# Kernel tuning notes

Hardware: AMD Instinct MI355X
Metric: run time of the kernel (lower is better)

Reference implementation:

```python
import jax, jax.numpy as jnp
import numpy as np

HIDDEN = 1024
HEAD_DIM = 64
N_HEADS = HIDDEN // HEAD_DIM  # 16
BATCH = 2
SEQ = 2048
ROT_DIM = HEAD_DIM // 2  # RotaryEmbedding(head_dim // 2): only first half of head dims rotated
THETA = 10000.0
SCALE_BASE = 512.0  # lucidrains xpos default
EPS = 1e-5


def setup_inputs() -> dict:
    key = jax.random.key(0)
    ks = jax.random.split(key, 8)

    def lin(k, shape, fan_in):
        b = 1.0 / np.sqrt(fan_in)
        return jax.random.uniform(k, shape, jnp.float32, -b, b)

    return {
        "x": jax.random.normal(ks[0], (BATCH, SEQ, HIDDEN), jnp.float32),
        "ln1_w": jnp.ones((HIDDEN,), jnp.float32),
        "ln1_b": jnp.zeros((HIDDEN,), jnp.float32),
        "wqkv_w": lin(ks[1], (HIDDEN, 3 * HIDDEN), HIDDEN),
        "wg_w": lin(ks[2], (HIDDEN, HIDDEN), HIDDEN),
        "wo_w": lin(ks[3], (HIDDEN, HIDDEN), HIDDEN),
        "gn_w": jnp.ones((N_HEADS,), jnp.float32),
        "gn_b": jnp.zeros((N_HEADS,), jnp.float32),
        "ln2_w": jnp.ones((HIDDEN,), jnp.float32),
        "ln2_b": jnp.zeros((HIDDEN,), jnp.float32),
        "w1_w": lin(ks[4], (HIDDEN, HIDDEN), HIDDEN),
        "w1_b": lin(ks[5], (HIDDEN,), HIDDEN),
        "w2_w": lin(ks[6], (HIDDEN, HIDDEN), HIDDEN),
        "w2_b": lin(ks[7], (HIDDEN,), HIDDEN),
    }


def _layernorm(x, w, b):
    m = jnp.mean(x, axis=-1, keepdims=True)
    v = jnp.mean(jnp.square(x - m), axis=-1, keepdims=True)
    return (x - m) * jax.lax.rsqrt(v + EPS) * w + b


def _rotate_half(x):
    # interleaved pairs: (d r) with r=2 -> (-x2, x1)
    xs = x.reshape(x.shape[:-1] + (ROT_DIM // 2, 2))
    x1, x2 = xs[..., 0], xs[..., 1]
    return jnp.stack((-x2, x1), axis=-1).reshape(x.shape)


def _xpos_rotary(q, k):
    # lucidrains RotaryEmbedding(dim=ROT_DIM, use_xpos=True).rotate_queries_and_keys
    S = q.shape[-2]
    half = jnp.arange(0, ROT_DIM, 2, dtype=jnp.float32)
    inv_freq = 1.0 / (THETA ** (half / ROT_DIM))          # [ROT_DIM/2]
    t = jnp.arange(S, dtype=jnp.float32)
    freqs = jnp.repeat(t[:, None] * inv_freq, 2, axis=-1)  # [S, ROT_DIM] interleaved
    scale_vals = (half + 0.4 * ROT_DIM) / (1.4 * ROT_DIM)  # [ROT_DIM/2]
    power = (t - S // 2) / SCALE_BASE
    scale = scale_vals[None, :] ** power[:, None]           # [S, ROT_DIM/2]
    scale = jnp.concatenate((scale, scale), axis=-1)        # [S, ROT_DIM] (cat, not interleave)
    cos, sin = jnp.cos(freqs), jnp.sin(freqs)

    def apply(x, sc):
        xl, xr = x[..., :ROT_DIM], x[..., ROT_DIM:]
        xl = xl * cos * sc + _rotate_half(xl) * sin * sc
        return jnp.concatenate((xl, xr), axis=-1)

    return apply(q, scale), apply(k, 1.0 / scale)


def _mish(x):
    return x * jnp.tanh(jax.nn.softplus(x))


def reference(x, ln1_w, ln1_b, wqkv_w, wg_w, wo_w, gn_w, gn_b,
              ln2_w, ln2_b, w1_w, w1_b, w2_w, w2_b):
    B, S, _ = x.shape
    h = _layernorm(x, ln1_w, ln1_b)

    # qkv: [B,S,3H] -> 'B S (H D) -> B H S D' with D = 3*head_dim, then chunk 3
    qkv = (h @ wqkv_w).reshape(B, S, N_HEADS, 3 * HEAD_DIM).transpose(0, 2, 1, 3)
    q, k, v = jnp.split(qkv, 3, axis=-1)  # each [B,H,S,head_dim]
    q, k = _xpos_rotary(q, k)

    # decay mask: gamma_h^(i-j) for i>=j (causal), 0 otherwise
    gamma = 1.0 - 2.0 ** (-5.0 - jnp.arange(N_HEADS, dtype=jnp.float32))
    idx = jnp.arange(S)
    nm = (idx[:, None] - idx[None, :]).astype(jnp.float32)     # [S,S]
    decay = jnp.where(nm >= 0, gamma[:, None, None] ** nm, 0.0)  # [H,S,S]

    ret = jnp.einsum('bhsd,bhtd->bhst', q, k) * decay[None]
    ret = jnp.einsum('bhst,bhtd->bhsd', ret, v)               # [B,H,S,head_dim]

    # GroupNorm(n_heads, n_heads): normalize each head over (S, head_dim)
    m = jnp.mean(ret, axis=(2, 3), keepdims=True)
    va = jnp.mean(jnp.square(ret - m), axis=(2, 3), keepdims=True)
    ret = (ret - m) * jax.lax.rsqrt(va + EPS)
    ret = ret * gn_w[None, :, None, None] + gn_b[None, :, None, None]

    y = ret.transpose(0, 2, 1, 3).reshape(B, S, HIDDEN)       # B H S D -> B S (H D)
    y = _mish(h @ wg_w) * y
    y = y @ wo_w

    y = y + x
    z = _layernorm(y, ln2_w, ln2_b)
    ffn = jax.nn.gelu(z @ w1_w + w1_b, approximate=False) @ w2_w + w2_b
    return ffn + y
```

## Files before the change

### kernel.cpp

```cpp
#include <hip/hip_runtime.h>


constexpr int S_LEN = 2048;
constexpr int HID   = 1024;
constexpr int NH    = 16;
constexpr int HD    = 64;
constexpr int BATCH = 2;
constexpr float EPS = 1e-5f;

using short8 = __attribute__((ext_vector_type(8))) short;
using f32x4  = __attribute__((ext_vector_type(4))) float;

__device__ __forceinline__ ushort bf16rne(float x) {
  unsigned u = __float_as_uint(x);
  unsigned r = (u + 0x7fffu + ((u >> 16) & 1u)) >> 16;
  return (ushort)r;
}
__device__ __forceinline__ void split2(float x, ushort& hi, ushort& lo) {
  hi = bf16rne(x);
  float hf = __uint_as_float((unsigned)hi << 16);
  lo = bf16rne(x - hf);
}

__device__ __forceinline__ void block_reduce2(float& s, float& ss) {
  #pragma unroll
  for (int o = 32; o > 0; o >>= 1) {
    s  += __shfl_down(s, o, 64);
    ss += __shfl_down(ss, o, 64);
  }
  __shared__ float ls[4], lss[4];
  const int lane = threadIdx.x & 63;
  const int w    = threadIdx.x >> 6;
  if (lane == 0) { ls[w] = s; lss[w] = ss; }
  __syncthreads();
  if (threadIdx.x == 0) {
    float a = 0.f, b2 = 0.f;
    #pragma unroll
    for (int i = 0; i < 4; ++i) { a += ls[i]; b2 += lss[i]; }
    ls[0] = a; lss[0] = b2;
  }
  __syncthreads();
  s = ls[0]; ss = lss[0];
}

__global__ __launch_bounds__(256) void ln_split_kernel(const float* __restrict__ x,
    const float* __restrict__ w, const float* __restrict__ b,
    ushort* __restrict__ oh, ushort* __restrict__ ol) {
  const int row = blockIdx.x;
  const int t   = threadIdx.x;
  const float4 v = reinterpret_cast<const float4*>(x + (size_t)row * HID)[t];
  float s  = v.x + v.y + v.z + v.w;
  float ss = v.x*v.x + v.y*v.y + v.z*v.z + v.w*v.w;
  block_reduce2(s, ss);
  const float mean = s * (1.f / HID);
  const float var  = ss * (1.f / HID) - mean * mean;
  const float rstd = rsqrtf(var + EPS);
  const float4 wv = reinterpret_cast<const float4*>(w)[t];
  const float4 bv = reinterpret_cast<const float4*>(b)[t];
  float o[4];
  o[0] = (v.x - mean) * rstd * wv.x + bv.x;
  o[1] = (v.y - mean) * rstd * wv.y + bv.y;
  o[2] = (v.z - mean) * rstd * wv.z + bv.z;
  o[3] = (v.w - mean) * rstd * wv.w + bv.w;
  ushort4 hv, lv;
  split2(o[0], hv.x, lv.x); split2(o[1], hv.y, lv.y);
  split2(o[2], hv.z, lv.z); split2(o[3], hv.w, lv.w);
  *reinterpret_cast<ushort4*>(oh + (size_t)row * HID + t * 4) = hv;
  *reinterpret_cast<ushort4*>(ol + (size_t)row * HID + t * 4) = lv;
}

__global__ __launch_bounds__(256) void wsplit_kernel(const float* __restrict__ W,
    ushort* __restrict__ Th, ushort* __restrict__ Tl, int N) {
  __shared__ float tile[32][33];
  const int k0 = blockIdx.y * 32;
  const int n0 = blockIdx.x * 32;
  const int tx = threadIdx.x & 31, ty = threadIdx.x >> 5;
  #pragma unroll
  for (int r = 0; r < 4; ++r)
    tile[ty + 8*r][tx] = W[(size_t)(k0 + ty + 8*r) * N + n0 + tx];
  __syncthreads();
  #pragma unroll
  for (int r = 0; r < 4; ++r) {
    const int n = ty + 8*r;
    const float v = tile[tx][n];
    ushort hi, lo; split2(v, hi, lo);
    Th[(size_t)(n0 + n) * 1024 + k0 + tx] = hi;
    Tl[(size_t)(n0 + n) * 1024 + k0 + tx] = lo;
  }
}

__global__ __launch_bounds__(256) void rot_tables_kernel(float* __restrict__ tcs,
    float* __restrict__ tsn, float* __restrict__ tscq, float* __restrict__ tsck) {
  const int g = blockIdx.x * 256 + threadIdx.x;
  const int m = g & 15, s = g >> 4;
  const float invf = exp2f(-((float)(2 * m) * (1.f / 32.f)) * 13.287712379549449f);
  const float ang = (float)s * invf;
  tcs[g] = cosf(ang);
  tsn[g] = sinf(ang);
  const float p  = ((float)s - 1024.f) * (1.f / 512.f);
  const float sv = (2.f * (float)m + 12.8f) * (1.f / 44.8f);
  const float l  = log2f(sv) * p;
  tscq[g] = exp2f(l);
  tsck[g] = exp2f(-l);
}

__device__ __forceinline__ float mishf(float v) {
  return v * tanhf(log1pf(expf(v)));
}
__device__ __forceinline__ float geluf(float v) {
  return 0.5f * v * (1.f + erff(v * 0.7071067811865475f));
}

template <int EPI, int BN>
__global__ __launch_bounds__(256, 2) void gemm_mfma(
    const ushort* __restrict__ Ah, const ushort* __restrict__ Al,
    const ushort* __restrict__ Bh, const ushort* __restrict__ Bl,
    const float* __restrict__ bias, const float* __restrict__ res,
    float* __restrict__ C, ushort* __restrict__ Ch, ushort* __restrict__ Cl,
    int N, int K) {
  constexpr int MI  = (BN == 128) ? 4 : 2;
  constexpr int BCH = BN / 32;
  __shared__ ushort sA[2][128 * 64];
  __shared__ ushort sB[2][BN * 64];
  const int tid  = threadIdx.x;
  const int lane = tid & 63;
  const int w    = tid >> 6;
  const int wm   = (BN == 128) ? (w >> 1) : w;
  const int wn   = (BN == 128) ? (w & 1)  : 0;
  const int rowBase = blockIdx.y * 128;
  const int colBase = blockIdx.x * BN;

  f32x4 acc[MI][4] = {};

  const int l8   = lane >> 3;
  const int kswz = ((lane & 7) * 16) ^ (l8 << 4);

  for (int k0 = 0; k0 < K; k0 += 64) {
    __syncthreads();
    #pragma unroll
    for (int c = 0; c < 4; ++c) {
      const int row = w * 32 + c * 8;
      const char* gah = (const char*)(Ah + (size_t)(rowBase + row + l8) * K + k0) + kswz;
      const char* gal = (const char*)(Al + (size_t)(rowBase + row + l8) * K + k0) + kswz;
      __builtin_amdgcn_global_load_lds((const __attribute__((address_space(1))) void*)gah,
          (__attribute__((address_space(3))) void*)((char*)sA[0] + row * 128), 16, 0, 0);
      __builtin_amdgcn_global_load_lds((const __attribute__((address_space(1))) void*)gal,
          (__attribute__((address_space(3))) void*)((char*)sA[1] + row * 128), 16, 0, 0);
    }
    #pragma unroll
    for (int c = 0; c < BCH; ++c) {
      const int row = w * (BN / 4) + c * 8;
      const char* gbh = (const char*)(Bh + (size_t)(colBase + row + l8) * K + k0) + kswz;
      const char* gbl = (const char*)(Bl + (size_t)(colBase + row + l8) * K + k0) + kswz;
      __builtin_amdgcn_global_load_lds((const __attribute__((address_space(1))) void*)gbh,
          (__attribute__((address_space(3))) void*)((char*)sB[0] + row * 128), 16, 0, 0);
      __builtin_amdgcn_global_load_lds((const __attribute__((address_space(1))) void*)gbl,
          (__attribute__((address_space(3))) void*)((char*)sB[1] + row * 128), 16, 0, 0);
    }
    __syncthreads();
    #pragma unroll
    for (int kk = 0; kk < 2; ++kk) {
      const int kb = kk * 64 + ((lane >> 4) << 4);
      short8 ah[MI], al[MI], bh[4], bl[4];
      #pragma unroll
      for (int i = 0; i < MI; ++i) {
        const int row = wm * (16 * MI) + i * 16 + (lane & 15);
        const int off = row * 128 + (kb ^ ((row & 7) << 4));
        ah[i] = *(const short8*)((const char*)sA[0] + off);
        al[i] = *(const short8*)((const char*)sA[1] + off);
      }
      #pragma unroll
      for (int j = 0; j < 4; ++j) {
        const int row = wn * 64 + j * 16 + (lane & 15);
        const int off = row * 128 + (kb ^ ((row & 7) << 4));
        bh[j] = *(const short8*)((const char*)sB[0] + off);
        bl[j] = *(const short8*)((const char*)sB[1] + off);
      }
      #pragma unroll
      for (int i = 0; i < MI; ++i)
        #pragma unroll
        for (int j = 0; j < 4; ++j) {
          acc[i][j] = __builtin_amdgcn_mfma_f32_16x16x32_bf16(ah[i], bh[j], acc[i][j], 0, 0, 0);
          acc[i][j] = __builtin_amdgcn_mfma_f32_16x16x32_bf16(ah[i], bl[j], acc[i][j], 0, 0, 0);
          acc[i][j] = __builtin_amdgcn_mfma_f32_16x16x32_bf16(al[i], bh[j], acc[i][j], 0, 0, 0);
        }
    }
  }

  const int cRow = rowBase + wm * (16 * MI) + ((lane >> 4) << 2);
  const int cCol = colBase + wn * 64 + (lane & 15);
  #pragma unroll
  for (int i = 0; i < MI; ++i)
    #pragma unroll
    for (int j = 0; j < 4; ++j) {
      const int gc = cCol + j * 16;
      #pragma unroll
      for (int r = 0; r < 4; ++r) {
        const int gr = cRow + i * 16 + r;
        float v = acc[i][j][r];
        if constexpr (EPI == 2) v += res[(size_t)gr * N + gc];
        if constexpr (EPI == 3) v = geluf(v + bias[gc]);
        if constexpr (EPI == 4) v += bias[gc] + res[(size_t)gr * N + gc];
        if constexpr (EPI == 3) {
          ushort hi, lo; split2(v, hi, lo);
          Ch[(size_t)gr * N + gc] = hi;
          Cl[(size_t)gr * N + gc] = lo;
        } else {
          C[(size_t)gr * N + gc] = v;
        }
      }
    }
}

__global__ __launch_bounds__(256, 2) void gemm_qkvg_rot(
    const ushort* __restrict__ Ah, const ushort* __restrict__ Al,
    const ushort* __restrict__ Bh, const ushort* __restrict__ Bl,
    const float* __restrict__ tcs, const float* __restrict__ tsn,
    const float* __restrict__ tscq, const float* __restrict__ tsck,
    ushort* __restrict__ qTh, ushort* __restrict__ qTl,
    ushort* __restrict__ kTh, ushort* __restrict__ kTl,
    ushort* __restrict__ vTh, ushort* __restrict__ vTl,
    float* __restrict__ gmish) {
  const int K = 1024;
  __shared__ ushort sA[2][128 * 64];
  __shared__ ushort sB[2][128 * 64];
  const int tid  = threadIdx.x;
  const int lane = tid & 63;
  const int w    = tid >> 6;
  const int wm   = w >> 1, wn = w & 1;
  const int rowBase = blockIdx.y * 128;
  const int colBase = blockIdx.x * 128;

  f32x4 acc[4][4] = {};

  const int l8   = lane >> 3;
  const int kswz = ((lane & 7) * 16) ^ (l8 << 4);

  for (int k0 = 0; k0 < K; k0 += 64) {
    __syncthreads();
    #pragma unroll
    for (int c = 0; c < 4; ++c) {
      const int row = w * 32 + c * 8;
      const char* gah = (const char*)(Ah + (size_t)(rowBase + row + l8) * K + k0) + kswz;
      const char* gal = (const char*)(Al + (size_t)(rowBase + row + l8) * K + k0) + kswz;
      const char* gbh = (const char*)(Bh + (size_t)(colBase + row + l8) * K + k0) + kswz;
      const char* gbl = (const char*)(Bl + (size_t)(colBase + row + l8) * K + k0) + kswz;
      __builtin_amdgcn_global_load_lds((const __attribute__((address_space(1))) void*)gah,
          (__attribute__((address_space(3))) void*)((char*)sA[0] + row * 128), 16, 0, 0);
      __builtin_amdgcn_global_load_lds((const __attribute__((address_space(1))) void*)gal,
          (__attribute__((address_space(3))) void*)((char*)sA[1] + row * 128), 16, 0, 0);
      __builtin_amdgcn_global_load_lds((const __attribute__((address_space(1))) void*)gbh,
          (__attribute__((address_space(3))) void*)((char*)sB[0] + row * 128), 16, 0, 0);
      __builtin_amdgcn_global_load_lds((const __attribute__((address_space(1))) void*)gbl,
          (__attribute__((address_space(3))) void*)((char*)sB[1] + row * 128), 16, 0, 0);
    }
    __syncthreads();
    #pragma unroll
    for (int kk = 0; kk < 2; ++kk) {
      const int kb = kk * 64 + ((lane >> 4) << 4);
      short8 ah[4], al[4], bh[4], bl[4];
      #pragma unroll
      for (int i = 0; i < 4; ++i) {
        const int row = wm * 64 + i * 16 + (lane & 15);
        const int off = row * 128 + (kb ^ ((row & 7) << 4));
        ah[i] = *(const short8*)((const char*)sA[0] + off);
        al[i] = *(const short8*)((const char*)sA[1] + off);
      }
      #pragma unroll
      for (int j = 0; j < 4; ++j) {
        const int row = wn * 64 + j * 16 + (lane & 15);
        const int off = row * 128 + (kb ^ ((row & 7) << 4));
        bh[j] = *(const short8*)((const char*)sB[0] + off);
        bl[j] = *(const short8*)((const char*)sB[1] + off);
      }
      #pragma unroll
      for (int i = 0; i < 4; ++i)
        #pragma unroll
        for (int j = 0; j < 4; ++j) {
          acc[i][j] = __builtin_amdgcn_mfma_f32_16x16x32_bf16(ah[i], bh[j], acc[i][j], 0, 0, 0);
          acc[i][j] = __builtin_amdgcn_mfma_f32_16x16x32_bf16(ah[i], bl[j], acc[i][j], 0, 0, 0);
          acc[i][j] = __builtin_amdgcn_mfma_f32_16x16x32_bf16(al[i], bh[j], acc[i][j], 0, 0, 0);
        }
    }
  }

  const int c0   = colBase + wn * 64;
  const int cRow = rowBase + wm * 64 + ((lane >> 4) << 2);
  const int lc   = lane & 15;

  if (c0 >= 3072) {
    const int gc0 = c0 - 3072;
    #pragma unroll
    for (int i = 0; i < 4; ++i)
      #pragma unroll
      for (int j = 0; j < 4; ++j) {
        const int gc = gc0 + j * 16 + lc;
        #pragma unroll
        for (int r = 0; r < 4; ++r) {
          const int gr = cRow + i * 16 + r;
          gmish[(size_t)gr * 1024 + gc] = mishf(acc[i][j][r]);
        }
      }
    return;
  }
  const int region = (c0 >> 6) % 3;
  const int hh     = c0 / 192;

  if (region == 2) {
    #pragma unroll
    for (int j = 0; j < 4; ++j) {
      const int d = 16 * j + lc;
      #pragma unroll
      for (int i = 0; i < 4; ++i) {
        const int s0g = cRow + i * 16;
        const int bb  = s0g >> 11;
        const int s0  = s0g & 2047;
        ushort4 hv, lv;
        #pragma unroll
        for (int r = 0; r < 4; ++r) {
          ushort hi, lo; split2(acc[i][j][r], hi, lo);
          ((ushort*)&hv)[r] = hi; ((ushort*)&lv)[r] = lo;
        }
        const size_t a = ((size_t)(bb * NH + hh) * HD + d) * S_LEN + s0;
        *reinterpret_cast<ushort4*>(vTh + a) = hv;
        *reinterpret_cast<ushort4*>(vTl + a) = lv;
      }
    }
  } else {
    ushort* Oh = (region == 0) ? qTh : kTh;
    ushort* Ol = (region == 0) ? qTl : kTl;
    const float* tsc = (region == 0) ? tscq : tsck;
    #pragma unroll
    for (int j = 0; j < 4; ++j) {
      const int d  = 16 * j + lc;
      const int ii = d >> 1;
      const int im = d & 15;
      #pragma unroll
      for (int i = 0; i < 4; ++i) {
        const int s0g = cRow + i * 16;
        const int bb  = s0g >> 11;
        #pragma unroll
        for (int r = 0; r < 4; ++r) {
          const int s = (s0g + r) & 2047;
          float v = acc[i][j][r];
          float p = __shfl_xor(v, 1);
          float resv;
          if (j < 2) {
            const float cs  = tcs[s * 16 + ii];
            const float sn  = tsn[s * 16 + ii];
            const float scl = tsc[s * 16 + im];
            resv = ((lane & 1) ? (v * cs + p * sn) : (v * cs - p * sn)) * scl;
          } else {
            resv = v;
          }
          ushort hi, lo; split2(resv, hi, lo);
          const size_t a = ((size_t)(bb * NH + hh) * S_LEN + s) * HD + d;
          Oh[a] = hi; Ol[a] = lo;
        }
      }
    }
  }
}

__global__ __launch_bounds__(256, 2) void retention_mfma(
    const ushort* __restrict__ qTh, const ushort* __restrict__ qTl,
    const ushort* __restrict__ kTh, const ushort* __restrict__ kTl,
    const ushort* __restrict__ vTh, const ushort* __restrict__ vTl,
    float* __restrict__ ret) {
  const int sblk = blockIdx.x, h = blockIdx.y, b = blockIdx.z;
  const int tid = threadIdx.x, lane = tid & 63, w = tid >> 6;
  const int sBase = sblk << 6;
  const float l2g = log2f(1.f - exp2f(-5.f - (float)h));

  __shared__ ushort Qh[4096], Ql[4096], Kh[4096], Kl[4096],
                    Vh[4096], Vl[4096], Sh[4096], Sl[4096];

  const int l8   = lane >> 3;
  const int kswz = ((lane & 7) * 16) ^ (l8 << 4);

  auto stage16 = [&](const ushort* src, int pitch, ushort* dst, int r0) {
    #pragma unroll
    for (int c = 0; c < 2; ++c) {
      const int row = r0 + c * 8;
      const char* g = (const char*)(src + (size_t)(row + l8) * pitch) + kswz;
      __builtin_amdgcn_global_load_lds((const __attribute__((address_space(1))) void*)g,
          (__attribute__((address_space(3))) void*)((char*)dst + row * 128), 16, 0, 0);
    }
  };

  const size_t bh  = (size_t)(b * NH + h);
  const size_t bho = bh * (S_LEN * HD);

  stage16(qTh + bho + (size_t)sBase * HD, 64, Qh, w * 16);
  stage16(qTl + bho + (size_t)sBase * HD, 64, Ql, w * 16);

  const int sQr = (lane >> 4) << 2;
  float gs[4], gti[4];
  #pragma unroll
  for (int r = 0; r < 4; ++r) gs[r] = exp2f(l2g * (float)(w * 16 + sQr + r));
  #pragma unroll
  for (int j = 0; j < 4; ++j) gti[j] = exp2f(-l2g * (float)((lane & 15) + 16 * j));

  f32x4 acc[4] = {};

  const int aRow = w * 16 + (lane & 15);
  const int aOff = aRow * 128;
  const int aswz = (aRow & 7) << 4;

  for (int tblk = 0; tblk <= sblk; ++tblk) {
    const int tBase = tblk << 6;
    const int nmin  = sBase - tBase - 63;
    if (nmin > 0 && (float)nmin * l2g < -45.f) continue;
    __syncthreads();
    stage16(kTh + bho + (size_t)tBase * HD, 64,   Kh, w * 16);
    stage16(kTl + bho + (size_t)tBase * HD, 64,   Kl, w * 16);
    stage16(vTh + bho + tBase,              2048, Vh, w * 16);
    stage16(vTl + bho + tBase,              2048, Vl, w * 16);
    __syncthreads();

    f32x4 sc[4] = {};
    #pragma unroll
    for (int ks = 0; ks < 2; ++ks) {
      const int kb = ks * 64 + ((lane >> 4) << 4);
      const short8 qhf = *(const short8*)((const char*)Qh + aOff + (kb ^ aswz));
      const short8 qlf = *(const short8*)((const char*)Ql + aOff + (kb ^ aswz));
      #pragma unroll
      for (int j = 0; j < 4; ++j) {
        const int br = j * 16 + (lane & 15);
        const int bo = br * 128 + (kb ^ ((br & 7) << 4));
        const short8 khf = *(const short8*)((const char*)Kh + bo);
        const short8 klf = *(const short8*)((const char*)Kl + bo);
        sc[j] = __builtin_amdgcn_mfma_f32_16x16x32_bf16(qhf, khf, sc[j], 0, 0, 0);
        sc[j] = __builtin_amdgcn_mfma_f32_16x16x32_bf16(qhf, klf, sc[j], 0, 0, 0);
        sc[j] = __builtin_amdgcn_mfma_f32_16x16x32_bf16(qlf, khf, sc[j], 0, 0, 0);
      }
    }

    const float D0  = exp2f(l2g * (float)(sBase - tBase));
    const bool diag = (tBase == sBase);
    #pragma unroll
    for (int j = 0; j < 4; ++j) {
      const int tLoc  = (lane & 15) + 16 * j;
      const float gj  = D0 * gti[j];
      #pragma unroll
      for (int r = 0; r < 4; ++r) {
        const int sLoc = w * 16 + sQr + r;
        float dec = gj * gs[r];
        if (diag && sLoc < tLoc) dec = 0.f;
        const float v = sc[j][r] * dec;
        ushort hi, lo; split2(v, hi, lo);
        const int off = sLoc * 128 + ((tLoc * 2) ^ ((sLoc & 7) << 4));
        *(ushort*)((char*)Sh + off) = hi;
        *(ushort*)((char*)Sl + off) = lo;
      }
    }
    __syncthreads();

    #pragma unroll
    for (int ks = 0; ks < 2; ++ks) {
      const int kb = ks * 64 + ((lane >> 4) << 4);
      const short8 shf = *(const short8*)((const char*)Sh + aOff + (kb ^ aswz));
      const short8 slf = *(const short8*)((const char*)Sl + aOff + (kb ^ aswz));
      #pragma unroll
      for (int j = 0; j < 4; ++j) {
        const int br = j * 16 + (lane & 15);
        const int bo = br * 128 + (kb ^ ((br & 7) << 4));
        const short8 vhf = *(const short8*)((const char*)Vh + bo);
        const short8 vlf = *(const short8*)((const char*)Vl + bo);
        acc[j] = __builtin_amdgcn_mfma_f32_16x16x32_bf16(shf, vhf, acc[j], 0, 0, 0);
        acc[j] = __builtin_amdgcn_mfma_f32_16x16x32_bf16(shf, vlf, acc[j], 0, 0, 0);
        acc[j] = __builtin_amdgcn_mfma_f32_16x16x32_bf16(slf, vhf, acc[j], 0, 0, 0);
      }
    }
  }

  float* ob = ret + (bh * S_LEN + sBase) * HD;
  #pragma unroll
  for (int j = 0; j < 4; ++j)
    #pragma unroll
    for (int r = 0; r < 4; ++r)
      ob[(w * 16 + sQr + r) * 64 + j * 16 + (lane & 15)] = acc[j][r];
}

__global__ __launch_bounds__(256) void gn_kernel(const float* __restrict__ ret,
    const float* __restrict__ gm, const float* __restrict__ gn_w, const float* __restrict__ gn_b,
    ushort* __restrict__ yh, ushort* __restrict__ yl) {
  const int bh = blockIdx.x;
  const int b = bh >> 4, h = bh & 15;
  const float4* r4 = reinterpret_cast<const float4*>(ret + (size_t)bh * (S_LEN * HD));
  float s = 0.f, ss = 0.f;
  for (int i = threadIdx.x; i < S_LEN * HD / 4; i += 256) {
    const float4 v = r4[i];
    s  += v.x + v.y + v.z + v.w;
    ss += v.x*v.x + v.y*v.y + v.z*v.z + v.w*v.w;
  }
  block_reduce2(s, ss);
  const float inv  = 1.f / (float)(S_LEN * HD);
  const float mean = s * inv;
  const float var  = ss * inv - mean * mean;
  const float rstd = rsqrtf(var + EPS);
  const float a = gn_w[h] * rstd;
  const float c = gn_b[h] - mean * a;
  for (int i = threadIdx.x; i < S_LEN * HD / 4; i += 256) {
    const float4 v = r4[i];
    const int e    = i << 2;
    const int srow = e >> 6;
    const int d    = e & 63;
    const size_t oidx = (size_t)(b * S_LEN + srow) * HID + h * HD + d;
    const float4 g = *reinterpret_cast<const float4*>(gm + oidx);
    float o0 = (v.x * a + c) * g.x;
    float o1 = (v.y * a + c) * g.y;
    float o2 = (v.z * a + c) * g.z;
    float o3 = (v.w * a + c) * g.w;
    ushort4 hv, lv;
    split2(o0, hv.x, lv.x); split2(o1, hv.y, lv.y);
    split2(o2, hv.z, lv.z); split2(o3, hv.w, lv.w);
    *reinterpret_cast<ushort4*>(yh + oidx) = hv;
    *reinterpret_cast<ushort4*>(yl + oidx) = lv;
  }
}

extern "C" void kernel_launch(void* const* d_in, const int* in_sizes, int n_in,
                              void* d_out, int out_size, void* d_ws, size_t ws_size,
                              hipStream_t stream) {
  const float* x     = (const float*)d_in[0];
  const float* ln1_w = (const float*)d_in[1];
  const float* ln1_b = (const float*)d_in[2];
  const float* wqkv  = (const float*)d_in[3];
  const float* wg    = (const float*)d_in[4];
  const float* wo    = (const float*)d_in[5];
  const float* gn_w  = (const float*)d_in[6];
  const float* gn_b  = (const float*)d_in[7];
  const float* ln2_w = (const float*)d_in[8];
  const float* ln2_b = (const float*)d_in[9];
  const float* w1    = (const float*)d_in[10];
  const float* w1_b  = (const float*)d_in[11];
  const float* w2    = (const float*)d_in[12];
  const float* w2_b  = (const float*)d_in[13];

  char* ws = (char*)d_ws;
  ushort* wqkvgT_h = (ushort*)(ws + 0);
  ushort* wqkvgT_l = (ushort*)(ws + 8388608);
  ushort* woT_h   = (ushort*)(ws + 16777216);
  ushort* woT_l   = (ushort*)(ws + 18874368);
  ushort* w1T_h   = (ushort*)(ws + 20971520);
  ushort* w1T_l   = (ushort*)(ws + 23068672);
  ushort* w2T_h   = (ushort*)(ws + 25165824);
  ushort* w2T_l   = (ushort*)(ws + 27262976);
  ushort* h_hi    = (ushort*)(ws + 29360128);
  ushort* h_lo    = (ushort*)(ws + 37748736);
  float*  tcs     = (float*) (ws + 46137344);
  float*  tsn     = (float*) (ws + 46268416);
  float*  tscq    = (float*) (ws + 46399488);
  float*  tsck    = (float*) (ws + 46530560);
  ushort* qT_h    = (ushort*)(ws + 46661632);
  ushort* qT_l    = (ushort*)(ws + 55050240);
  ushort* kT_h    = (ushort*)(ws + 63438848);
  ushort* kT_l    = (ushort*)(ws + 71827456);
  ushort* vT_h    = (ushort*)(ws + 80216064);
  ushort* vT_l    = (ushort*)(ws + 88604672);
  float*  gmish   = (float*) (ws + 96993280);
  float*  ret     = (float*) (ws + 29360128);
  ushort* yin_h   = (ushort*)(ws + 46661632);
  ushort* yin_l   = (ushort*)(ws + 55050240);
  float*  y       = (float*) (ws + 63438848);
  ushort* z_h     = (ushort*)(ws + 80216064);
  ushort* z_l     = (ushort*)(ws + 88604672);
  ushort* f_h     = (ushort*)(ws + 96993280);
  ushort* f_l     = (ushort*)(ws + 105381888);
  float*  out     = (float*)d_out;

  wsplit_kernel<<<dim3(3072/32, 32), 256, 0, stream>>>(wqkv, wqkvgT_h, wqkvgT_l, 3072);
  wsplit_kernel<<<dim3(1024/32, 32), 256, 0, stream>>>(wg, wqkvgT_h + 3072*1024, wqkvgT_l + 3072*1024, 1024);
  wsplit_kernel<<<dim3(1024/32, 32), 256, 0, stream>>>(wo, woT_h, woT_l, 1024);
  wsplit_kernel<<<dim3(1024/32, 32), 256, 0, stream>>>(w1, w1T_h, w1T_l, 1024);
  wsplit_kernel<<<dim3(1024/32, 32), 256, 0, stream>>>(w2, w2T_h, w2T_l, 1024);
  rot_tables_kernel<<<128, 256, 0, stream>>>(tcs, tsn, tscq, tsck);

  ln_split_kernel<<<BATCH * S_LEN, 256, 0, stream>>>(x, ln1_w, ln1_b, h_hi, h_lo);
  gemm_qkvg_rot<<<dim3(4096/128, 4096/128), 256, 0, stream>>>(h_hi, h_lo, wqkvgT_h, wqkvgT_l,
      tcs, tsn, tscq, tsck, qT_h, qT_l, kT_h, kT_l, vT_h, vT_l, gmish);
  retention_mfma<<<dim3(S_LEN/64, NH, BATCH), 256, 0, stream>>>(qT_h, qT_l, kT_h, kT_l,
      vT_h, vT_l, ret);
  gn_kernel<<<BATCH * NH, 256, 0, stream>>>(ret, gmish, gn_w, gn_b, yin_h, yin_l);
  gemm_mfma<2, 64><<<dim3(1024/64, 4096/128), 256, 0, stream>>>(yin_h, yin_l, woT_h, woT_l,
      nullptr, x, y, nullptr, nullptr, 1024, 1024);
  ln_split_kernel<<<BATCH * S_LEN, 256, 0, stream>>>(y, ln2_w, ln2_b, z_h, z_l);
  gemm_mfma<3, 64><<<dim3(1024/64, 4096/128), 256, 0, stream>>>(z_h, z_l, w1T_h, w1T_l,
      w1_b, nullptr, nullptr, f_h, f_l, 1024, 1024);
  gemm_mfma<4, 64><<<dim3(1024/64, 4096/128), 256, 0, stream>>>(f_h, f_l, w2T_h, w2T_l,
      w2_b, y, out, nullptr, nullptr, 1024, 1024);
}
```

Before: 582.0 us.

## Remap block indices for XCD-aware locality, hold Q in registers, raise occupancy

All GEMM and retention launches become 1D grids whose block index is permuted so consecutive blocks on each of the 8 XCDs share A/B tiles or heads in L2. Retention now processes long causal rows first. It also loads Q fragments straight into registers instead of staging them through LDS, which cuts LDS use so occupancy can rise to 3 blocks per CU. The GEMM is specialised to BN=64, and launch bounds go to 3 waves-per-EU hints, which risks register spills.

```diff
diff --git a/kernel.cpp b/kernel.cpp
--- a/kernel.cpp
+++ b/kernel.cpp
@@ -111,24 +111,26 @@
   return 0.5f * v * (1.f + erff(v * 0.7071067811865475f));
 }
 
-template <int EPI, int BN>
-__global__ __launch_bounds__(256, 2) void gemm_mfma(
+template <int EPI>
+__global__ __launch_bounds__(256, 3) void gemm_mfma(
     const ushort* __restrict__ Ah, const ushort* __restrict__ Al,
     const ushort* __restrict__ Bh, const ushort* __restrict__ Bl,
     const float* __restrict__ bias, const float* __restrict__ res,
     float* __restrict__ C, ushort* __restrict__ Ch, ushort* __restrict__ Cl,
     int N, int K) {
-  constexpr int MI  = (BN == 128) ? 4 : 2;
-  constexpr int BCH = BN / 32;
+  constexpr int BN = 64;
+  constexpr int MI = 2;
   __shared__ ushort sA[2][128 * 64];
   __shared__ ushort sB[2][BN * 64];
+  const int D = blockIdx.x;
+  const int L = (D & 7) * 64 + (D >> 3);
+  const int bix = L & 15, biy = L >> 4;
   const int tid  = threadIdx.x;
   const int lane = tid & 63;
   const int w    = tid >> 6;
-  const int wm   = (BN == 128) ? (w >> 1) : w;
-  const int wn   = (BN == 128) ? (w & 1)  : 0;
-  const int rowBase = blockIdx.y * 128;
-  const int colBase = blockIdx.x * BN;
+  const int wm   = w, wn = 0;
+  const int rowBase = biy * 128;
+  const int colBase = bix * BN;
 
   f32x4 acc[MI][4] = {};
 
@@ -148,8 +150,8 @@
           (__attribute__((address_space(3))) void*)((char*)sA[1] + row * 128), 16, 0, 0);
     }
     #pragma unroll
-    for (int c = 0; c < BCH; ++c) {
-      const int row = w * (BN / 4) + c * 8;
+    for (int c = 0; c < 2; ++c) {
+      const int row = w * 16 + c * 8;
       const char* gbh = (const char*)(Bh + (size_t)(colBase + row + l8) * K + k0) + kswz;
       const char* gbl = (const char*)(Bl + (size_t)(colBase + row + l8) * K + k0) + kswz;
       __builtin_amdgcn_global_load_lds((const __attribute__((address_space(1))) void*)gbh,
@@ -224,12 +226,15 @@
   const int K = 1024;
   __shared__ ushort sA[2][128 * 64];
   __shared__ ushort sB[2][128 * 64];
+  const int D = blockIdx.x;
+  const int L = (D & 7) * 128 + (D >> 3);
+  const int bix = L & 31, biy = L >> 5;
   const int tid  = threadIdx.x;
   const int lane = tid & 63;
   const int w    = tid >> 6;
   const int wm   = w >> 1, wn = w & 1;
-  const int rowBase = blockIdx.y * 128;
-  const int colBase = blockIdx.x * 128;
+  const int rowBase = biy * 128;
+  const int colBase = bix * 128;
 
   f32x4 acc[4][4] = {};
 
@@ -362,18 +367,21 @@
   }
 }
 
-__global__ __launch_bounds__(256, 2) void retention_mfma(
+__global__ __launch_bounds__(256, 3) void retention_mfma(
     const ushort* __restrict__ qTh, const ushort* __restrict__ qTl,
     const ushort* __restrict__ kTh, const ushort* __restrict__ kTl,
     const ushort* __restrict__ vTh, const ushort* __restrict__ vTl,
     float* __restrict__ ret) {
-  const int sblk = blockIdx.x, h = blockIdx.y, b = blockIdx.z;
+  const int D = blockIdx.x;
+  const int L = (D & 7) * 128 + (D >> 3);
+  const int sblk = 31 - (L & 31);
+  const int h = (L >> 5) & 15;
+  const int b = L >> 9;
   const int tid = threadIdx.x, lane = tid & 63, w = tid >> 6;
   const int sBase = sblk << 6;
   const float l2g = log2f(1.f - exp2f(-5.f - (float)h));
 
-  __shared__ ushort Qh[4096], Ql[4096], Kh[4096], Kl[4096],
-                    Vh[4096], Vl[4096], Sh[4096], Sl[4096];
+  __shared__ ushort Kh[4096], Kl[4096], Vh[4096], Vl[4096], Sh[4096], Sl[4096];
 
   const int l8   = lane >> 3;
   const int kswz = ((lane & 7) * 16) ^ (l8 << 4);
@@ -391,8 +399,17 @@
   const size_t bh  = (size_t)(b * NH + h);
   const size_t bho = bh * (S_LEN * HD);
 
-  stage16(qTh + bho + (size_t)sBase * HD, 64, Qh, w * 16);
-  stage16(qTl + bho + (size_t)sBase * HD, 64, Ql, w * 16);
+  short8 qh[2], ql[2];
+  {
+    const int qrow = sBase + w * 16 + (lane & 15);
+    const int d0   = (lane >> 4) << 3;
+    const ushort* qb = qTh + bho + (size_t)qrow * HD;
+    const ushort* qc = qTl + bho + (size_t)qrow * HD;
+    qh[0] = *(const short8*)(qb + d0);
+    qh[1] = *(const short8*)(qb + 32 + d0);
+    ql[0] = *(const short8*)(qc + d0);
+    ql[1] = *(const short8*)(qc + 32 + d0);
+  }
 
   const int sQr = (lane >> 4) << 2;
   float gs[4], gti[4];
@@ -422,17 +439,15 @@
     #pragma unroll
     for (int ks = 0; ks < 2; ++ks) {
       const int kb = ks * 64 + ((lane >> 4) << 4);
-      const short8 qhf = *(const short8*)((const char*)Qh + aOff + (kb ^ aswz));
-      const short8 qlf = *(const short8*)((const char*)Ql + aOff + (kb ^ aswz));
       #pragma unroll
       for (int j = 0; j < 4; ++j) {
         const int br = j * 16 + (lane & 15);
         const int bo = br * 128 + (kb ^ ((br & 7) << 4));
         const short8 khf = *(const short8*)((const char*)Kh + bo);
         const short8 klf = *(const short8*)((const char*)Kl + bo);
-        sc[j] = __builtin_amdgcn_mfma_f32_16x16x32_bf16(qhf, khf, sc[j], 0, 0, 0);
-        sc[j] = __builtin_amdgcn_mfma_f32_16x16x32_bf16(qhf, klf, sc[j], 0, 0, 0);
-        sc[j] = __builtin_amdgcn_mfma_f32_16x16x32_bf16(qlf, khf, sc[j], 0, 0, 0);
+        sc[j] = __builtin_amdgcn_mfma_f32_16x16x32_bf16(qh[ks], khf, sc[j], 0, 0, 0);
+        sc[j] = __builtin_amdgcn_mfma_f32_16x16x32_bf16(qh[ks], klf, sc[j], 0, 0, 0);
+        sc[j] = __builtin_amdgcn_mfma_f32_16x16x32_bf16(ql[ks], khf, sc[j], 0, 0, 0);
       }
     }
 
@@ -578,16 +593,15 @@
   rot_tables_kernel<<<128, 256, 0, stream>>>(tcs, tsn, tscq, tsck);
 
   ln_split_kernel<<<BATCH * S_LEN, 256, 0, stream>>>(x, ln1_w, ln1_b, h_hi, h_lo);
-  gemm_qkvg_rot<<<dim3(4096/128, 4096/128), 256, 0, stream>>>(h_hi, h_lo, wqkvgT_h, wqkvgT_l,
+  gemm_qkvg_rot<<<1024, 256, 0, stream>>>(h_hi, h_lo, wqkvgT_h, wqkvgT_l,
       tcs, tsn, tscq, tsck, qT_h, qT_l, kT_h, kT_l, vT_h, vT_l, gmish);
-  retention_mfma<<<dim3(S_LEN/64, NH, BATCH), 256, 0, stream>>>(qT_h, qT_l, kT_h, kT_l,
-      vT_h, vT_l, ret);
+  retention_mfma<<<1024, 256, 0, stream>>>(qT_h, qT_l, kT_h, kT_l, vT_h, vT_l, ret);
   gn_kernel<<<BATCH * NH, 256, 0, stream>>>(ret, gmish, gn_w, gn_b, yin_h, yin_l);
-  gemm_mfma<2, 64><<<dim3(1024/64, 4096/128), 256, 0, stream>>>(yin_h, yin_l, woT_h, woT_l,
+  gemm_mfma<2><<<512, 256, 0, stream>>>(yin_h, yin_l, woT_h, woT_l,
       nullptr, x, y, nullptr, nullptr, 1024, 1024);
   ln_split_kernel<<<BATCH * S_LEN, 256, 0, stream>>>(y, ln2_w, ln2_b, z_h, z_l);
-  gemm_mfma<3, 64><<<dim3(1024/64, 4096/128), 256, 0, stream>>>(z_h, z_l, w1T_h, w1T_l,
+  gemm_mfma<3><<<512, 256, 0, stream>>>(z_h, z_l, w1T_h, w1T_l,
       w1_b, nullptr, nullptr, f_h, f_l, 1024, 1024);
-  gemm_mfma<4, 64><<<dim3(1024/64, 4096/128), 256, 0, stream>>>(f_h, f_l, w2T_h, w2T_l,
+  gemm_mfma<4><<<512, 256, 0, stream>>>(f_h, f_l, w2T_h, w2T_l,
       w2_b, y, out, nullptr, nullptr, 1024, 1024);
 }
```

New measurement: 550.6 us. 1.06x faster.
